# Optimization experiments

Hardware: AMD Instinct MI355X
Metric: run time of the kernel (lower is better)

## Reference

```python
import jax, jax.numpy as jnp
import numpy as np

NUM_CP = 5      # num_control_points per edge
DEGREE = 3      # B-spline degree


def bspline_basis(x, n, d):
    """Cox-de Boor B-spline basis.
    x: [B, I] inputs; returns [B, I, n] basis values.
    Uniform knots on [-1, 1], length n + d + 1."""
    t = jnp.linspace(-1.0, 1.0, n + d + 1).astype(x.dtype)
    x_ = x[..., None]                       # [B, I, 1]
    # degree-0 indicator basis: [B, I, n+d]
    B = ((x_ >= t[:-1]) & (x_ < t[1:])).astype(x.dtype)
    for r in range(1, d + 1):
        m = n + d - r                       # number of basis funcs at this level
        left = (x_ - t[:m]) / (t[r:r + m] - t[:m]) * B[..., :m]
        right = (t[r + 1:r + 1 + m] - x_) / (t[r + 1:r + 1 + m] - t[1:1 + m]) * B[..., 1:m + 1]
        B = left + right
    return B                                # [B, I, n]


def setup_inputs() -> dict:
    key = jax.random.key(0)
    k1, k2, k3 = jax.random.split(key, 3)
    batch, input_dim, output_dim = 4096, 1024, 1024
    x = jax.random.uniform(k1, (batch, input_dim), dtype=jnp.float32)
    coeffs = jax.random.normal(k2, (input_dim, output_dim, NUM_CP), dtype=jnp.float32)
    importance = jax.random.normal(k3, (input_dim, output_dim), dtype=jnp.float32)
    return {"x": x, "coeffs": coeffs, "importance": importance}


def reference(x, coeffs, importance):
    # basis: [B, I, K]; per-edge spline weights scaled by importance: [I, O, K]
    basis = bspline_basis(x, NUM_CP, DEGREE)
    w = importance[..., None] * coeffs
    # out[b, o] = sum_{i,k} basis[b,i,k] * w[i,o,k]
    out = jnp.einsum('bik,iok->bo', basis, w)
    return out
```

## Files before the change

kernel.cpp:

```cpp
#include <hip/hip_runtime.h>
#include <stdint.h>

#define B_DIM 4096
#define I_DIM 1024
#define O_DIM 1024
#define KD    4096
#define OUT_N (B_DIM * O_DIM)

#define SPLITK 4
#define KCHUNK (KD / SPLITK)
#define NKT    (KCHUNK / 64)

typedef short v8s __attribute__((ext_vector_type(8)));
typedef float v4f __attribute__((ext_vector_type(4)));

__device__ __forceinline__ uint16_t f2bf(float f) {
    union { float f; uint32_t u; } v; v.f = f;
    uint32_t u = v.u;
    return (uint16_t)((u + 0x7FFFu + ((u >> 16) & 1u)) >> 16);
}
__device__ __forceinline__ float bf2f(uint32_t hi_bits) {
    union { uint32_t u; float f; } v; v.u = hi_bits; return v.f;
}

__device__ __forceinline__ void gload_lds16(const uint16_t* g, uint16_t* l) {
    __builtin_amdgcn_global_load_lds(
        (const __attribute__((address_space(1))) void*)g,
        (__attribute__((address_space(3))) void*)l,
        16, 0, 0);
}

__global__ void zero_kernel(float4* __restrict__ out, int n4) {
    int idx = blockIdx.x * blockDim.x + threadIdx.x;
    if (idx < n4) out[idx] = float4{0.f, 0.f, 0.f, 0.f};
}

__global__ void prep_kernel(const float* __restrict__ x,
                            const float* __restrict__ coeffs,
                            const float* __restrict__ imp,
                            uint16_t* __restrict__ A, uint16_t* __restrict__ WT) {
    __shared__ __align__(16) char lds[65536];
    int id = blockIdx.x;
    int t  = threadIdx.x;
    if (id < 512) {
        int b0 = id * 8;
#pragma unroll
        for (int bb = 0; bb < 8; ++bb) {
            int b = b0 + bb;
#pragma unroll
            for (int q = 0; q < 4; ++q) {
                int i = q * 256 + t;
                float xv = x[(size_t)b * I_DIM + i];
                float tt = 4.0f * xv;
                float fj = floorf(tt);
                fj = fminf(fmaxf(fj, 0.0f), 3.0f);
                int j4 = (int)fj;
                float u  = tt - fj;
                float um = 1.0f - u;
                float u2 = u * u, u3 = u2 * u;
                const float s = 1.0f / 6.0f;
                float w0 = um * um * um * s;
                float w1 = (3.0f * u3 - 6.0f * u2 + 4.0f) * s;
                float w2 = (-3.0f * u3 + 3.0f * u2 + 3.0f * u + 1.0f) * s;
                float w3 = u3 * s;
                float o0 = (j4 == 0) ? w0 : 0.0f;
                float o1 = (j4 == 0) ? w1 : (j4 == 1) ? w0 : 0.0f;
                float o2 = (j4 == 0) ? w2 : (j4 == 1) ? w1 : (j4 == 2) ? w0 : 0.0f;
                float o3 = (j4 == 0) ? w3 : (j4 == 1) ? w2 : (j4 == 2) ? w1 : w0;
                union { uint16_t h[4]; uint2 v; } pk;
                pk.h[0] = f2bf(o0); pk.h[1] = f2bf(o1);
                pk.h[2] = f2bf(o2); pk.h[3] = f2bf(o3);
                *(uint2*)(A + (size_t)b * KD + (size_t)i * 4) = pk.v;
            }
        }
    } else {
        int bid = id - 512;
        int i0 = (bid & 31) * 32;
        int o0 = (bid >> 5) * 256;
        int o  = o0 + t;
        const int swz = (t & 7) << 4;
        union { uint16_t h[8]; uint4 v; } pk;
#pragma unroll
        for (int ii = 0; ii < 32; ++ii) {
            int i = i0 + ii;
            float im = imp[(size_t)i * O_DIM + o];
            const float* cp = coeffs + ((size_t)i * O_DIM + o) * 5;
            int base = (ii & 1) * 4;
            pk.h[base + 0] = f2bf(im * cp[1]);
            pk.h[base + 1] = f2bf(im * cp[2]);
            pk.h[base + 2] = f2bf(im * cp[3]);
            pk.h[base + 3] = f2bf(im * cp[4]);
            if (ii & 1)
                *(uint4*)(lds + t * 256 + (((ii - 1) * 8) ^ swz)) = pk.v;
        }
        __syncthreads();
#pragma unroll
        for (int j = 0; j < 16; ++j) {
            int c   = t + 256 * j;
            int row = c >> 4;
            int u   = c & 15;
            uint4 v = *(const uint4*)(lds + row * 256 + ((u * 16) ^ ((row & 7) << 4)));
            *(uint4*)(WT + (size_t)(o0 + row) * KD + i0 * 4 + u * 8) = v;
        }
    }
}


template<int RH>
__device__ __forceinline__ void read_half_a(const uint16_t* base, int lane, v8s (&f)[4][2]) {
    const char* b = (const char*)base;
    const int swz = (lane & 7) << 4;
    const int kb0 = (lane >> 4) << 4;
    const int lr0 = RH * 64 + (lane & 15);
#pragma unroll
    for (int mb = 0; mb < 4; ++mb)
#pragma unroll
        for (int ks = 0; ks < 2; ++ks)
            f[mb][ks] = *(const v8s*)(b + (size_t)(lr0 + mb * 16) * 128 + ((kb0 + ks * 64) ^ swz));
}

template<int CH>
__device__ __forceinline__ void read_half_b(const uint16_t* base, int lane, int wchalf,
                                            v8s (&f)[2][2]) {
    const char* b = (const char*)base;
    const int swz = (lane & 7) << 4;
    const int kb0 = (lane >> 4) << 4;
    const int lo0 = wchalf + CH * 32 + (lane & 15);
#pragma unroll
    for (int nb = 0; nb < 2; ++nb)
#pragma unroll
        for (int ks = 0; ks < 2; ++ks)
            f[nb][ks] = *(const v8s*)(b + (size_t)(lo0 + nb * 16) * 128 + ((kb0 + ks * 64) ^ swz));
}

__device__ __forceinline__ void mma_q(const v8s (&a)[4][2], const v8s (&bq)[2][2],
                                      v4f (&ac)[4][2]) {
    __builtin_amdgcn_s_setprio(1);
#pragma unroll
    for (int mb = 0; mb < 4; ++mb)
#pragma unroll
        for (int nb = 0; nb < 2; ++nb)
#pragma unroll
            for (int ks = 0; ks < 2; ++ks)
                ac[mb][nb] = __builtin_amdgcn_mfma_f32_16x16x32_bf16(a[mb][ks], bq[nb][ks],
                                                                     ac[mb][nb], 0, 0, 0);
    __builtin_amdgcn_s_setprio(0);
}

template<int PARTIAL>
__global__ __launch_bounds__(512, 2)
void gemm_kernel(const uint16_t* __restrict__ A, const uint16_t* __restrict__ WT,
                 float* __restrict__ out, uint16_t* __restrict__ P) {
    int hw  = blockIdx.x;
    int lid = (hw & 7) * 32 + (hw >> 3);
    int nt = lid & 3, mt = (lid >> 2) & 15, sk = lid >> 6;

    int t    = threadIdx.x;
    int lane = t & 63;
    int wid  = t >> 6;
    int wr = wid >> 2, wc = wid & 3;

    __shared__ uint16_t sA[2][2][128 * 64];
    __shared__ uint16_t sB[2][2][128 * 64];

    const uint16_t* Ab = A  + (size_t)(mt * 256) * KD + sk * KCHUNK;
    const uint16_t* Bb = WT + (size_t)(nt * 256) * KD + sk * KCHUNK;

    const int r0  = t >> 3;
    const int kel = ((((t & 7) << 4) ^ ((r0 & 7) << 4)) >> 1);

    auto stageA = [&](int buf, int half, int kt) {
        const uint16_t* g = Ab + (size_t)(half * 128 + r0) * KD + kt * 64 + kel;
        gload_lds16(g,                   &sA[buf][half][t * 8]);
        gload_lds16(g + (size_t)64 * KD, &sA[buf][half][4096 + t * 8]);
    };
    auto stageB = [&](int buf, int half, int kt) {
        const uint16_t* g = Bb + (size_t)(half * 128 + r0) * KD + kt * 64 + kel;
        gload_lds16(g,                   &sB[buf][half][t * 8]);
        gload_lds16(g + (size_t)64 * KD, &sB[buf][half][4096 + t * 8]);
    };

    v8s af[4][2], bf0[2][2], bf1[2][2];
    v4f a00[4][2] = {}, a01[4][2] = {}, a10[4][2] = {}, a11[4][2] = {};

    const int wch = (wc & 1) * 64;
    const int bh  = wc >> 1;

    stageB(0, 0, 0); stageB(0, 1, 0);
    stageA(0, 0, 0); stageA(0, 1, 0);
    stageB(1, 0, 1); stageB(1, 1, 1);
    asm volatile("s_waitcnt vmcnt(4)" ::: "memory");
    __builtin_amdgcn_s_barrier();

#pragma unroll 2
    for (int g = 0; g < NKT; ++g) {
        const int buf = g & 1, nbuf = buf ^ 1;
        read_half_a<0>(&sA[buf][wr][0], lane, af);
        read_half_b<0>(&sB[buf][bh][0], lane, wch, bf0);
        if (g + 1 < NKT) stageA(nbuf, 0, g + 1);
        __builtin_amdgcn_s_barrier();
        asm volatile("s_waitcnt lgkmcnt(0)" ::: "memory");
        mma_q(af, bf0, a00);
        __builtin_amdgcn_s_barrier();

        read_half_b<1>(&sB[buf][bh][0], lane, wch, bf1);
        if (g + 1 < NKT) stageA(nbuf, 1, g + 1);
        __builtin_amdgcn_s_barrier();
        asm volatile("s_waitcnt lgkmcnt(0)" ::: "memory");
        mma_q(af, bf1, a01);
        __builtin_amdgcn_s_barrier();

        read_half_a<1>(&sA[buf][wr][0], lane, af);
        if (g + 2 < NKT) stageB(buf, 0, g + 2);
        __builtin_amdgcn_s_barrier();
        asm volatile("s_waitcnt lgkmcnt(0)" ::: "memory");
        mma_q(af, bf0, a10);
        __builtin_amdgcn_s_barrier();

        if (g + 2 < NKT) stageB(buf, 1, g + 2);
        __builtin_amdgcn_s_barrier();
        mma_q(af, bf1, a11);
        if (g < NKT - 2)       asm volatile("s_waitcnt vmcnt(4)" ::: "memory");
        else if (g == NKT - 2) asm volatile("s_waitcnt vmcnt(0)" ::: "memory");
        __builtin_amdgcn_s_barrier();
    }

    const int oc  = lane & 15;
    const int orr = (lane >> 4) * 4;
    if (PARTIAL) {
        uint16_t* pb = P + (size_t)sk * OUT_N
                         + (size_t)(mt * 256 + wr * 128) * O_DIM + nt * 256 + wc * 64;
#pragma unroll
        for (int mb = 0; mb < 4; ++mb)
#pragma unroll
            for (int nb = 0; nb < 2; ++nb)
#pragma unroll
                for (int r = 0; r < 4; ++r) {
                    pb[(size_t)(mb * 16 + orr + r) * O_DIM + nb * 16 + oc]           = f2bf(a00[mb][nb][r]);
                    pb[(size_t)(mb * 16 + orr + r) * O_DIM + 32 + nb * 16 + oc]      = f2bf(a01[mb][nb][r]);
                    pb[(size_t)(64 + mb * 16 + orr + r) * O_DIM + nb * 16 + oc]      = f2bf(a10[mb][nb][r]);
                    pb[(size_t)(64 + mb * 16 + orr + r) * O_DIM + 32 + nb * 16 + oc] = f2bf(a11[mb][nb][r]);
                }
    } else {
        float* ob = out + (size_t)(mt * 256 + wr * 128) * O_DIM + nt * 256 + wc * 64;
#pragma unroll
        for (int mb = 0; mb < 4; ++mb)
#pragma unroll
            for (int nb = 0; nb < 2; ++nb)
#pragma unroll
                for (int r = 0; r < 4; ++r) {
                    atomicAdd(&ob[(size_t)(mb * 16 + orr + r) * O_DIM + nb * 16 + oc],           a00[mb][nb][r]);
                    atomicAdd(&ob[(size_t)(mb * 16 + orr + r) * O_DIM + 32 + nb * 16 + oc],      a01[mb][nb][r]);
                    atomicAdd(&ob[(size_t)(64 + mb * 16 + orr + r) * O_DIM + nb * 16 + oc],      a10[mb][nb][r]);
                    atomicAdd(&ob[(size_t)(64 + mb * 16 + orr + r) * O_DIM + 32 + nb * 16 + oc], a11[mb][nb][r]);
                }
    }
}

__global__ void reduce_kernel(const uint16_t* __restrict__ P, float* __restrict__ out) {
    size_t idx = ((size_t)blockIdx.x * 256 + threadIdx.x) * 8;
    float s[8] = {0, 0, 0, 0, 0, 0, 0, 0};
#pragma unroll
    for (int sk = 0; sk < SPLITK; ++sk) {
        uint4 v = *(const uint4*)(P + (size_t)sk * OUT_N + idx);
        uint32_t w[4] = {v.x, v.y, v.z, v.w};
#pragma unroll
        for (int j = 0; j < 4; ++j) {
            s[2 * j]     += bf2f((w[j] & 0xFFFFu) << 16);
            s[2 * j + 1] += bf2f(w[j] & 0xFFFF0000u);
        }
    }
    float4 lo = {s[0], s[1], s[2], s[3]};
    float4 hi = {s[4], s[5], s[6], s[7]};
    *(float4*)(out + idx)     = lo;
    *(float4*)(out + idx + 4) = hi;
}

extern "C" void kernel_launch(void* const* d_in, const int* in_sizes, int n_in,
                              void* d_out, int out_size, void* d_ws, size_t ws_size,
                              hipStream_t stream) {
    const float* x      = (const float*)d_in[0];
    const float* coeffs = (const float*)d_in[1];
    const float* imp    = (const float*)d_in[2];
    float* out = (float*)d_out;

    const size_t A_ELEMS  = (size_t)B_DIM * KD;
    const size_t WT_ELEMS = (size_t)O_DIM * KD;
    const size_t P_ELEMS  = (size_t)SPLITK * OUT_N;
    uint16_t* A  = (uint16_t*)d_ws;
    uint16_t* WT = A + A_ELEMS;
    uint16_t* P  = WT + WT_ELEMS;
    const size_t need = (A_ELEMS + WT_ELEMS + P_ELEMS) * 2;

    hipLaunchKernelGGL(prep_kernel, dim3(512 + 128), dim3(256), 0, stream,
                       x, coeffs, imp, A, WT);
    if (ws_size >= need) {
        hipLaunchKernelGGL((gemm_kernel<1>), dim3(256), dim3(512), 0, stream, A, WT, out, P);
        hipLaunchKernelGGL(reduce_kernel, dim3(OUT_N / 8 / 256), dim3(256), 0, stream, P, out);
    } else {
        hipLaunchKernelGGL(zero_kernel, dim3((OUT_N / 4) / 256), dim3(256), 0, stream,
                           (float4*)out, OUT_N / 4);
        hipLaunchKernelGGL((gemm_kernel<0>), dim3(256), dim3(512), 0, stream, A, WT, out, P);
    }
}
```

Baseline: 64.34 us.

## Fuse split-K reduction into GEMM via last-arriving-block counter

Removes the separate reduce kernel. Each GEMM block writes its bf16 partial tile, fences, and increments a per-tile counter that is zeroed by an extra block in the prep kernel. The last of the four split-K blocks then sums all partials for that tile and writes fp32 output. This saves one kernel launch and lets the reduction overlap with other GEMM blocks. In exchange, the final reduction work is concentrated in 64 blocks, and the added fences and a syncthreads could serialize the tail.

```diff
diff --git a/kernel.cpp b/kernel.cpp
--- a/kernel.cpp
+++ b/kernel.cpp
@@ -38,7 +38,8 @@
 __global__ void prep_kernel(const float* __restrict__ x,
                             const float* __restrict__ coeffs,
                             const float* __restrict__ imp,
-                            uint16_t* __restrict__ A, uint16_t* __restrict__ WT) {
+                            uint16_t* __restrict__ A, uint16_t* __restrict__ WT,
+                            int* __restrict__ cnt) {
     __shared__ __align__(16) char lds[65536];
     int id = blockIdx.x;
     int t  = threadIdx.x;
@@ -73,7 +74,7 @@
                 *(uint2*)(A + (size_t)b * KD + (size_t)i * 4) = pk.v;
             }
         }
-    } else {
+    } else if (id < 640) {
         int bid = id - 512;
         int i0 = (bid & 31) * 32;
         int o0 = (bid >> 5) * 256;
@@ -102,6 +103,8 @@
             uint4 v = *(const uint4*)(lds + row * 256 + ((u * 16) ^ ((row & 7) << 4)));
             *(uint4*)(WT + (size_t)(o0 + row) * KD + i0 * 4 + u * 8) = v;
         }
+    } else {
+        if (t < 64) cnt[t] = 0;
     }
 }
 
@@ -150,7 +153,7 @@
 template<int PARTIAL>
 __global__ __launch_bounds__(512, 2)
 void gemm_kernel(const uint16_t* __restrict__ A, const uint16_t* __restrict__ WT,
-                 float* __restrict__ out, uint16_t* __restrict__ P) {
+                 float* __restrict__ out, uint16_t* __restrict__ P, int* __restrict__ cnt) {
     int hw  = blockIdx.x;
     int lid = (hw & 7) * 32 + (hw >> 3);
     int nt = lid & 3, mt = (lid >> 2) & 15, sk = lid >> 6;
@@ -241,6 +244,39 @@
                     pb[(size_t)(64 + mb * 16 + orr + r) * O_DIM + nb * 16 + oc]      = f2bf(a10[mb][nb][r]);
                     pb[(size_t)(64 + mb * 16 + orr + r) * O_DIM + 32 + nb * 16 + oc] = f2bf(a11[mb][nb][r]);
                 }
+        __threadfence();
+        __shared__ int is_last;
+        if (t == 0) {
+            int old = atomicAdd(&cnt[mt * 4 + nt], 1);
+            is_last = (old == SPLITK - 1);
+        }
+        __syncthreads();
+        if (is_last) {
+            __threadfence();
+            const size_t tbase = (size_t)(mt * 256) * O_DIM + nt * 256;
+#pragma unroll 4
+            for (int j = 0; j < 16; ++j) {
+                int e   = (j * 512 + t) * 8;
+                int row = e >> 8;
+                int col = e & 255;
+                size_t off = tbase + (size_t)row * O_DIM + col;
+                float s[8] = {0, 0, 0, 0, 0, 0, 0, 0};
+#pragma unroll
+                for (int s2 = 0; s2 < SPLITK; ++s2) {
+                    uint4 v = *(const uint4*)(P + (size_t)s2 * OUT_N + off);
+                    uint32_t w[4] = {v.x, v.y, v.z, v.w};
+#pragma unroll
+                    for (int q = 0; q < 4; ++q) {
+                        s[2 * q]     += bf2f((w[q] & 0xFFFFu) << 16);
+                        s[2 * q + 1] += bf2f(w[q] & 0xFFFF0000u);
+                    }
+                }
+                float4 lo = {s[0], s[1], s[2], s[3]};
+                float4 hi = {s[4], s[5], s[6], s[7]};
+                *(float4*)(out + off)     = lo;
+                *(float4*)(out + off + 4) = hi;
+            }
+        }
     } else {
         float* ob = out + (size_t)(mt * 256 + wr * 128) * O_DIM + nt * 256 + wc * 64;
 #pragma unroll
@@ -257,25 +293,6 @@
     }
 }
 
-__global__ void reduce_kernel(const uint16_t* __restrict__ P, float* __restrict__ out) {
-    size_t idx = ((size_t)blockIdx.x * 256 + threadIdx.x) * 8;
-    float s[8] = {0, 0, 0, 0, 0, 0, 0, 0};
-#pragma unroll
-    for (int sk = 0; sk < SPLITK; ++sk) {
-        uint4 v = *(const uint4*)(P + (size_t)sk * OUT_N + idx);
-        uint32_t w[4] = {v.x, v.y, v.z, v.w};
-#pragma unroll
-        for (int j = 0; j < 4; ++j) {
-            s[2 * j]     += bf2f((w[j] & 0xFFFFu) << 16);
-            s[2 * j + 1] += bf2f(w[j] & 0xFFFF0000u);
-        }
-    }
-    float4 lo = {s[0], s[1], s[2], s[3]};
-    float4 hi = {s[4], s[5], s[6], s[7]};
-    *(float4*)(out + idx)     = lo;
-    *(float4*)(out + idx + 4) = hi;
-}
-
 extern "C" void kernel_launch(void* const* d_in, const int* in_sizes, int n_in,
                               void* d_out, int out_size, void* d_ws, size_t ws_size,
                               hipStream_t stream) {
@@ -290,16 +307,16 @@
     uint16_t* A  = (uint16_t*)d_ws;
     uint16_t* WT = A + A_ELEMS;
     uint16_t* P  = WT + WT_ELEMS;
-    const size_t need = (A_ELEMS + WT_ELEMS + P_ELEMS) * 2;
-
-    hipLaunchKernelGGL(prep_kernel, dim3(512 + 128), dim3(256), 0, stream,
-                       x, coeffs, imp, A, WT);
+    int*      cnt = (int*)(P + P_ELEMS);
+    const size_t need = (A_ELEMS + WT_ELEMS + P_ELEMS) * 2 + 64 * 4;
+
+    hipLaunchKernelGGL(prep_kernel, dim3(512 + 128 + 1), dim3(256), 0, stream,
+                       x, coeffs, imp, A, WT, cnt);
     if (ws_size >= need) {
-        hipLaunchKernelGGL((gemm_kernel<1>), dim3(256), dim3(512), 0, stream, A, WT, out, P);
-        hipLaunchKernelGGL(reduce_kernel, dim3(OUT_N / 8 / 256), dim3(256), 0, stream, P, out);
+        hipLaunchKernelGGL((gemm_kernel<1>), dim3(256), dim3(512), 0, stream, A, WT, out, P, cnt);
     } else {
         hipLaunchKernelGGL(zero_kernel, dim3((OUT_N / 4) / 256), dim3(256), 0, stream,
                            (float4*)out, OUT_N / 4);
-        hipLaunchKernelGGL((gemm_kernel<0>), dim3(256), dim3(512), 0, stream, A, WT, out, P);
+        hipLaunchKernelGGL((gemm_kernel<0>), dim3(256), dim3(512), 0, stream, A, WT, out, P, cnt);
     }
 }
```

Measured after the change: 170.2 us. 164% more time.

## Shrink GEMM tile to 256x128 and halve split-K factor

Applied to the files above, without the earlier changes.

Changes the GEMM block tile from 256x256 to 256x128 output and reduces split-K from 4 to 2, keeping the total block count the same. Each block now runs twice as many K iterations with half the B staging and half the accumulators, which cuts register pressure and partial-sum traffic in the reduce step. The cost is lower arithmetic intensity per block, so more A data is reloaded across N tiles.

```diff
diff --git a/kernel.cpp b/kernel.cpp
--- a/kernel.cpp
+++ b/kernel.cpp
@@ -7,7 +7,7 @@
 #define KD    4096
 #define OUT_N (B_DIM * O_DIM)
 
-#define SPLITK 4
+#define SPLITK 2
 #define KCHUNK (KD / SPLITK)
 #define NKT    (KCHUNK / 64)
 
@@ -119,13 +119,11 @@
             f[mb][ks] = *(const v8s*)(b + (size_t)(lr0 + mb * 16) * 128 + ((kb0 + ks * 64) ^ swz));
 }
 
-template<int CH>
-__device__ __forceinline__ void read_half_b(const uint16_t* base, int lane, int wchalf,
-                                            v8s (&f)[2][2]) {
+__device__ __forceinline__ void read_b(const uint16_t* base, int lane, int wch, v8s (&f)[2][2]) {
     const char* b = (const char*)base;
     const int swz = (lane & 7) << 4;
     const int kb0 = (lane >> 4) << 4;
-    const int lo0 = wchalf + CH * 32 + (lane & 15);
+    const int lo0 = wch + (lane & 15);
 #pragma unroll
     for (int nb = 0; nb < 2; ++nb)
 #pragma unroll
@@ -153,7 +151,7 @@
                  float* __restrict__ out, uint16_t* __restrict__ P) {
     int hw  = blockIdx.x;
     int lid = (hw & 7) * 32 + (hw >> 3);
-    int nt = lid & 3, mt = (lid >> 2) & 15, sk = lid >> 6;
+    int nt = lid & 7, mt = (lid >> 3) & 15, sk = lid >> 7;
 
     int t    = threadIdx.x;
     int lane = t & 63;
@@ -161,10 +159,10 @@
     int wr = wid >> 2, wc = wid & 3;
 
     __shared__ uint16_t sA[2][2][128 * 64];
-    __shared__ uint16_t sB[2][2][128 * 64];
+    __shared__ uint16_t sB[2][2][64 * 64];
 
     const uint16_t* Ab = A  + (size_t)(mt * 256) * KD + sk * KCHUNK;
-    const uint16_t* Bb = WT + (size_t)(nt * 256) * KD + sk * KCHUNK;
+    const uint16_t* Bb = WT + (size_t)(nt * 128) * KD + sk * KCHUNK;
 
     const int r0  = t >> 3;
     const int kel = ((((t & 7) << 4) ^ ((r0 & 7) << 4)) >> 1);
@@ -175,52 +173,38 @@
         gload_lds16(g + (size_t)64 * KD, &sA[buf][half][4096 + t * 8]);
     };
     auto stageB = [&](int buf, int half, int kt) {
-        const uint16_t* g = Bb + (size_t)(half * 128 + r0) * KD + kt * 64 + kel;
-        gload_lds16(g,                   &sB[buf][half][t * 8]);
-        gload_lds16(g + (size_t)64 * KD, &sB[buf][half][4096 + t * 8]);
+        const uint16_t* g = Bb + (size_t)(half * 64 + r0) * KD + kt * 64 + kel;
+        gload_lds16(g, &sB[buf][half][t * 8]);
     };
 
-    v8s af[4][2], bf0[2][2], bf1[2][2];
-    v4f a00[4][2] = {}, a01[4][2] = {}, a10[4][2] = {}, a11[4][2] = {};
-
-    const int wch = (wc & 1) * 64;
+    v8s af[4][2], bf[2][2];
+    v4f aq0[4][2] = {}, aq1[4][2] = {};
+
+    const int wch = (wc & 1) * 32;
     const int bh  = wc >> 1;
 
     stageB(0, 0, 0); stageB(0, 1, 0);
     stageA(0, 0, 0); stageA(0, 1, 0);
     stageB(1, 0, 1); stageB(1, 1, 1);
-    asm volatile("s_waitcnt vmcnt(4)" ::: "memory");
+    asm volatile("s_waitcnt vmcnt(2)" ::: "memory");
     __builtin_amdgcn_s_barrier();
 
 #pragma unroll 2
     for (int g = 0; g < NKT; ++g) {
         const int buf = g & 1, nbuf = buf ^ 1;
         read_half_a<0>(&sA[buf][wr][0], lane, af);
-        read_half_b<0>(&sB[buf][bh][0], lane, wch, bf0);
-        if (g + 1 < NKT) stageA(nbuf, 0, g + 1);
+        read_b(&sB[buf][bh][0], lane, wch, bf);
+        if (g + 1 < NKT) { stageA(nbuf, 0, g + 1); stageA(nbuf, 1, g + 1); }
         __builtin_amdgcn_s_barrier();
         asm volatile("s_waitcnt lgkmcnt(0)" ::: "memory");
-        mma_q(af, bf0, a00);
-        __builtin_amdgcn_s_barrier();
-
-        read_half_b<1>(&sB[buf][bh][0], lane, wch, bf1);
-        if (g + 1 < NKT) stageA(nbuf, 1, g + 1);
+        mma_q(af, bf, aq0);
+        __builtin_amdgcn_s_barrier();
+        read_half_a<1>(&sA[buf][wr][0], lane, af);
+        if (g + 2 < NKT) { stageB(buf, 0, g + 2); stageB(buf, 1, g + 2); }
         __builtin_amdgcn_s_barrier();
         asm volatile("s_waitcnt lgkmcnt(0)" ::: "memory");
-        mma_q(af, bf1, a01);
-        __builtin_amdgcn_s_barrier();
-
-        read_half_a<1>(&sA[buf][wr][0], lane, af);
-        if (g + 2 < NKT) stageB(buf, 0, g + 2);
-        __builtin_amdgcn_s_barrier();
-        asm volatile("s_waitcnt lgkmcnt(0)" ::: "memory");
-        mma_q(af, bf0, a10);
-        __builtin_amdgcn_s_barrier();
-
-        if (g + 2 < NKT) stageB(buf, 1, g + 2);
-        __builtin_amdgcn_s_barrier();
-        mma_q(af, bf1, a11);
-        if (g < NKT - 2)       asm volatile("s_waitcnt vmcnt(4)" ::: "memory");
+        mma_q(af, bf, aq1);
+        if (g < NKT - 2)       asm volatile("s_waitcnt vmcnt(2)" ::: "memory");
         else if (g == NKT - 2) asm volatile("s_waitcnt vmcnt(0)" ::: "memory");
         __builtin_amdgcn_s_barrier();
     }
@@ -229,30 +213,26 @@
     const int orr = (lane >> 4) * 4;
     if (PARTIAL) {
         uint16_t* pb = P + (size_t)sk * OUT_N
-                         + (size_t)(mt * 256 + wr * 128) * O_DIM + nt * 256 + wc * 64;
+                         + (size_t)(mt * 256 + wr * 128) * O_DIM + nt * 128 + wc * 32;
 #pragma unroll
         for (int mb = 0; mb < 4; ++mb)
 #pragma unroll
             for (int nb = 0; nb < 2; ++nb)
 #pragma unroll
                 for (int r = 0; r < 4; ++r) {
-                    pb[(size_t)(mb * 16 + orr + r) * O_DIM + nb * 16 + oc]           = f2bf(a00[mb][nb][r]);
-                    pb[(size_t)(mb * 16 + orr + r) * O_DIM + 32 + nb * 16 + oc]      = f2bf(a01[mb][nb][r]);
-                    pb[(size_t)(64 + mb * 16 + orr + r) * O_DIM + nb * 16 + oc]      = f2bf(a10[mb][nb][r]);
-                    pb[(size_t)(64 + mb * 16 + orr + r) * O_DIM + 32 + nb * 16 + oc] = f2bf(a11[mb][nb][r]);
+                    pb[(size_t)(mb * 16 + orr + r) * O_DIM + nb * 16 + oc]      = f2bf(aq0[mb][nb][r]);
+                    pb[(size_t)(64 + mb * 16 + orr + r) * O_DIM + nb * 16 + oc] = f2bf(aq1[mb][nb][r]);
                 }
     } else {
-        float* ob = out + (size_t)(mt * 256 + wr * 128) * O_DIM + nt * 256 + wc * 64;
+        float* ob = out + (size_t)(mt * 256 + wr * 128) * O_DIM + nt * 128 + wc * 32;
 #pragma unroll
         for (int mb = 0; mb < 4; ++mb)
 #pragma unroll
             for (int nb = 0; nb < 2; ++nb)
 #pragma unroll
                 for (int r = 0; r < 4; ++r) {
-                    atomicAdd(&ob[(size_t)(mb * 16 + orr + r) * O_DIM + nb * 16 + oc],           a00[mb][nb][r]);
-                    atomicAdd(&ob[(size_t)(mb * 16 + orr + r) * O_DIM + 32 + nb * 16 + oc],      a01[mb][nb][r]);
-                    atomicAdd(&ob[(size_t)(64 + mb * 16 + orr + r) * O_DIM + nb * 16 + oc],      a10[mb][nb][r]);
-                    atomicAdd(&ob[(size_t)(64 + mb * 16 + orr + r) * O_DIM + 32 + nb * 16 + oc], a11[mb][nb][r]);
+                    atomicAdd(&ob[(size_t)(mb * 16 + orr + r) * O_DIM + nb * 16 + oc],      aq0[mb][nb][r]);
+                    atomicAdd(&ob[(size_t)(64 + mb * 16 + orr + r) * O_DIM + nb * 16 + oc], aq1[mb][nb][r]);
                 }
     }
 }
```

Measured after the change: 66.28 us. 1.03x slower.
